# Performance work log

Hardware: AMD Instinct MI355X
Metric: run time of the kernel (lower is better)

The kernel has to match this reference:

```python
import jax, jax.numpy as jnp
import numpy as np

B = 1024
IN_SIZ = 16384
OUT_SIZ = 16384
C = 8          # channel_siz
NLVL = 10
IFS = IN_SIZ // 2 ** NLVL                                   # 16, in_filter_siz
KLVL = min(int(np.floor(np.log2(OUT_SIZ / 2))), NLVL)       # 10
OFS = OUT_SIZ // 2 ** KLVL                                  # 16, out_filter_siz
STD = 0.9


def setup_inputs() -> dict:
    key = jax.random.key(0)
    ks = jax.random.split(key, 2 * NLVL + 3)
    inp = {}
    inp["x"] = jax.random.normal(ks[0], (B, IN_SIZ, 1), jnp.float32)
    inp["in_filter"] = jax.random.normal(ks[1], (IFS, 1, C), jnp.float32) * STD
    inp["in_bias"] = jnp.zeros((C,), jnp.float32)
    for lvl in range(1, NLVL + 1):
        k = 2 ** lvl
        inp[f"W{lvl}"] = jax.random.normal(ks[2 * lvl], (k, 2, C, C), jnp.float32) * STD
        inp[f"b{lvl}"] = jnp.zeros((k, C), jnp.float32)
    inp["fea_dense"] = jax.random.normal(ks[-1], (2 ** KLVL, C, OFS), jnp.float32) * STD
    return inp


def _level(v, W, b):
    # v: [Kp, B, L, C] parent branches; W: [2*Kp, 2, C, C]; b: [2*Kp, C]
    # kernel-2 stride-2 conv1d: out[t] = relu(x[2t] @ W[0] + x[2t+1] @ W[1] + b)
    Kp, Bn, L, Cc = v.shape
    xp = v.reshape(Kp, Bn, L // 2, 2, Cc)
    xr = jnp.repeat(xp, 2, axis=0)  # child itk reads parent itk // 2
    y = jnp.einsum('kbtsc,kscd->kbtd', xr, W) + b[:, None, None, :]
    return jax.nn.relu(y)


def reference(x, in_filter, in_bias,
              W1, b1, W2, b2, W3, b3, W4, b4, W5, b5,
              W6, b6, W7, b7, W8, b8, W9, b9, W10, b10,
              fea_dense):
    Ws = [W1, W2, W3, W4, W5, W6, W7, W8, W9, W10]
    bs = [b1, b2, b3, b4, b5, b6, b7, b8, b9, b10]
    Bn = x.shape[0]
    # input conv1d: kernel=IFS, stride=IFS (non-overlapping) == blocked matmul
    xin = x[..., 0].reshape(Bn, 2 ** NLVL, IFS)                       # [B, 1024, 16]
    v = jax.nn.relu(jnp.einsum('bnf,fc->bnc', xin, in_filter[:, 0, :]) + in_bias)
    v = v[None]                                                        # [1, B, 1024, C]
    for lvl in range(NLVL):  # klvl == nlvl: all levels branch (tree doubling)
        v = _level(v, Ws[lvl], bs[lvl])
    # v: [2^klvl, B, 1, C] -> per-branch dense feature map
    out = jnp.einsum('kbc,kcf->bkf', v[:, :, 0, :], fea_dense)         # [B, 1024, OFS]
    return out.reshape(Bn, OUT_SIZ, 1)
```

## Files before the change

kernel.cpp:

```cpp
#include <hip/hip_runtime.h>

struct PrepPtrs {
  const float* W[7]; const float* Bv[7]; const float* F; const float* fb;
  const float* W8; const float* B8; const float* W9; const float* B9;
  const float* W10; const float* B10;
};

__device__ __forceinline__ int cz(int c) { return c ^ ((c >> 3) & 3); }

__device__ __forceinline__ float4 relu4(float4 a) {
  return make_float4(fmaxf(a.x,0.f), fmaxf(a.y,0.f), fmaxf(a.z,0.f), fmaxf(a.w,0.f));
}
__device__ __forceinline__ void fma4(float4& acc, float s, const float4& wv) {
  acc.x = fmaf(s, wv.x, acc.x); acc.y = fmaf(s, wv.y, acc.y);
  acc.z = fmaf(s, wv.z, acc.z); acc.w = fmaf(s, wv.w, acc.w);
}
__device__ __forceinline__ float4 add4(float4 a, float4 b) {
  return make_float4(a.x+b.x, a.y+b.y, a.z+b.z, a.w+b.w);
}

__device__ __forceinline__ float4 entApply(const float4* __restrict__ e4,
                                           float4 A0, float4 A1,
                                           float4 C0, float4 C1) {
  float4 a0 = e4[16];
  float4 a1 = make_float4(0.f, 0.f, 0.f, 0.f);
  float4 a2 = make_float4(0.f, 0.f, 0.f, 0.f);
  float4 a3 = make_float4(0.f, 0.f, 0.f, 0.f);
  fma4(a0, A0.x, e4[0]);  fma4(a1, A0.y, e4[1]);  fma4(a2, A0.z, e4[2]);  fma4(a3, A0.w, e4[3]);
  fma4(a0, A1.x, e4[4]);  fma4(a1, A1.y, e4[5]);  fma4(a2, A1.z, e4[6]);  fma4(a3, A1.w, e4[7]);
  fma4(a0, C0.x, e4[8]);  fma4(a1, C0.y, e4[9]);  fma4(a2, C0.z, e4[10]); fma4(a3, C0.w, e4[11]);
  fma4(a0, C1.x, e4[12]); fma4(a1, C1.y, e4[13]); fma4(a2, C1.z, e4[14]); fma4(a3, C1.w, e4[15]);
  return relu4(add4(add4(a0, a1), add4(a2, a3)));
}

__global__ void bfly_prep(PrepPtrs P, float* __restrict__ wt) {
  int e = blockIdx.x * 256 + threadIdx.x;
  if (e >= 4094 * 68) return;
  int ent = e / 68, r = e % 68, dd = r & 3;
  const float* Ws; const float* Bs; int th;
  if (ent < 62) {
    if (ent < 60) {
      int lvl, base;
      if (ent < 4)       { lvl = 1; base = 0;  }
      else if (ent < 12) { lvl = 2; base = 4;  }
      else if (ent < 28) { lvl = 3; base = 12; }
      else               { lvl = 4; base = 28; }
      int k = (ent - base) >> 1; th = ent & 1;
      Ws = P.W[lvl-1] + k*128; Bs = P.Bv[lvl-1] + k*8;
    } else {
      th = ent - 60; Ws = P.F; Bs = P.fb;
    }
  } else if (ent < 510) {
    int eb = ent - 62;
    int q = eb / 56, rem = eb % 56;
    int lvl, Kl, base;
    if (rem < 8)       { lvl = 5; Kl = 4;  base = 0;  }
    else if (rem < 24) { lvl = 6; Kl = 8;  base = 8;  }
    else               { lvl = 7; Kl = 16; base = 24; }
    int rr = rem - base; int lk = rr >> 1; th = rr & 1;
    int kg = q * Kl + lk;
    Ws = P.W[lvl-1] + kg*128; Bs = P.Bv[lvl-1] + kg*8;
  } else if (ent < 1022) {
    int ec = ent - 510; int k = ec >> 1; th = ec & 1;
    Ws = P.W8 + k*128; Bs = P.B8 + k*8;
  } else if (ent < 2046) {
    int ec = ent - 1022; int k = ec >> 1; th = ec & 1;
    Ws = P.W9 + k*128; Bs = P.B9 + k*8;
  } else {
    int ec = ent - 2046; int k = ec >> 1; th = ec & 1;
    Ws = P.W10 + k*128; Bs = P.B10 + k*8;
  }
  float v;
  if (r < 64) { int s = r >> 5, c = (r >> 2) & 7; v = Ws[s*64 + c*8 + th*4 + dd]; }
  else v = Bs[th*4 + dd];
  wt[ent * 80 + r] = v;
}

__global__ __launch_bounds__(256, 2) void bfly_ka(
    const float* __restrict__ x, const float* __restrict__ wt,
    float* __restrict__ st1)
{
  const int tid = threadIdx.x;
  const int T = tid & 127;
  const int bb = tid >> 7;
  const int b = blockIdx.x * 2 + bb;
  const float4* wt4 = (const float4*)wt;
  const float4* xb4 = (const float4*)x + (size_t)b * 4096 + T * 32;

  float4 s[16], n[16];

#pragma unroll
  for (int th = 0; th < 2; ++th) {
    const float4* e4 = wt4 + (60 + th) * 20;
#pragma unroll
    for (int r = 0; r < 8; ++r) {
      float4 x0 = xb4[r*4], x1 = xb4[r*4+1], x2 = xb4[r*4+2], x3 = xb4[r*4+3];
      s[r*2+th] = entApply(e4, x0, x1, x2, x3);
    }
  }
#pragma unroll
  for (int th = 0; th < 2; ++th)
#pragma unroll
    for (int k = 0; k < 2; ++k) {
      const float4* e4 = wt4 + (0 + k*2 + th) * 20;
#pragma unroll
      for (int t = 0; t < 4; ++t)
        n[(k*4+t)*2+th] = entApply(e4, s[(2*t)*2], s[(2*t)*2+1],
                                       s[(2*t+1)*2], s[(2*t+1)*2+1]);
    }
#pragma unroll
  for (int th = 0; th < 2; ++th)
#pragma unroll
    for (int k = 0; k < 4; ++k) {
      const float4* e4 = wt4 + (4 + k*2 + th) * 20;
      const int kp = k >> 1;
#pragma unroll
      for (int t = 0; t < 2; ++t)
        s[(k*2+t)*2+th] = entApply(e4, n[(kp*4+2*t)*2], n[(kp*4+2*t)*2+1],
                                       n[(kp*4+2*t+1)*2], n[(kp*4+2*t+1)*2+1]);
    }
#pragma unroll
  for (int th = 0; th < 2; ++th)
#pragma unroll
    for (int k = 0; k < 8; ++k) {
      const float4* e4 = wt4 + (12 + k*2 + th) * 20;
      const int kp = k >> 1;
      n[k*2+th] = entApply(e4, s[(kp*2)*2], s[(kp*2)*2+1],
                               s[(kp*2+1)*2], s[(kp*2+1)*2+1]);
    }
  float4* o4 = (float4*)st1;
#pragma unroll
  for (int k = 0; k < 8; ++k)
#pragma unroll
    for (int th = 0; th < 2; ++th)
      o4[((size_t)(k*2+th) * 1024 + b) * 128 + T] = n[k*2+th];
}

template<int LV>
__device__ __forceinline__ void kb_level2(float4* __restrict__ s,
                                          const float4* __restrict__ wb4,
                                          int lane, int w) {
  constexpr int Tc = 1 << (10 - LV);
  constexpr int entB = (LV == 5) ? 0 : (LV == 6) ? 8 : 24;
  int kp, bl, t;
  if constexpr (LV == 5)      { kp = w >> 2; bl = ((w & 3) << 1) | (lane >> 5); t = lane & 31; }
  else if constexpr (LV == 6) { kp = w >> 1; bl = ((w & 1) << 2) | (lane >> 4); t = lane & 15; }
  else                        { kp = w;      bl = lane >> 3;                    t = lane & 7;  }
  const int pb = bl * 256 + kp * (2 * Tc) + 2 * t;
  const int cb = cz(pb);
  const int cb1 = cb ^ 1;
  float4 A0 = s[cb],       C0 = s[cb1];
  float4 A1 = s[cb + 128], C1 = s[cb1 + 128];
#pragma unroll
  for (int kk = 0; kk < 2; ++kk) {
    float4* pD = s + cz(bl * 256 + (2 * kp + kk) * Tc + t);
#pragma unroll
    for (int th = 0; th < 2; ++th) {
      const float4* e4 = wb4 + (entB + (2 * kp + kk) * 2 + th) * 20;
      pD[th * 128] = entApply(e4, A0, A1, C0, C1);
    }
  }
}

__global__ __launch_bounds__(512, 3) void bfly_kb(
    const float* __restrict__ st1, const float* __restrict__ wt,
    float* __restrict__ st2)
{
  __shared__ float4 s0[2048];
  const int tid = threadIdx.x;
  const int q = blockIdx.x, bt = blockIdx.y;
  const int lane = tid & 63;
  const int w = __builtin_amdgcn_readfirstlane(tid >> 6);
  const float4* wt4 = (const float4*)wt;
  const float4* wb4 = wt4 + 1240 + q * 56 * 20;
  const float4* i4 = (const float4*)st1;

#pragma unroll
  for (int it = 0; it < 4; ++it) {
    int o = tid + it * 512;
    int t3 = o & 127, h = (o >> 7) & 1, bl = o >> 8;
    float4 v = i4[((size_t)(q * 2 + h) * 1024 + bt * 8 + bl) * 128 + t3];
    s0[cz(bl * 256 + h * 128 + t3)] = v;
  }
  __syncthreads();
  {
    const float4* eb = wt4 + (28 + 4 * q) * 20;
    int bl = w, t = lane;
    int pb = bl * 256 + 2 * t;
    int cb = cz(pb), cb1 = cb ^ 1;
    float4 A0 = s0[cb], C0 = s0[cb1], A1 = s0[cb + 128], C1 = s0[cb1 + 128];
#pragma unroll
    for (int kk = 0; kk < 2; ++kk) {
      float4* pD = s0 + cz(bl * 256 + kk * 64 + t);
#pragma unroll
      for (int th = 0; th < 2; ++th) {
        const float4* e4 = eb + (kk * 2 + th) * 20;
        pD[th * 128] = entApply(e4, A0, A1, C0, C1);
      }
    }
  }
  __syncthreads();
  kb_level2<5>(s0, wb4, lane, w); __syncthreads();
  kb_level2<6>(s0, wb4, lane, w); __syncthreads();
  kb_level2<7>(s0, wb4, lane, w); __syncthreads();

  float4* o4 = (float4*)st2;
#pragma unroll
  for (int it = 0; it < 4; ++it) {
    int o = tid + it * 512;
    int bl = o & 7, t7 = (o >> 3) & 7, h = (o >> 6) & 1, lk7 = o >> 7;
    float4 v = s0[cz(bl * 256 + h * 128 + lk7 * 8 + t7)];
    o4[((size_t)((16 * q + lk7) * 8 + t7) * 2 + h) * 1024 + bt * 8 + bl] = v;
  }
}

__global__ __launch_bounds__(512, 2) void bfly_kc(
    const float* __restrict__ st, const float* __restrict__ wt,
    const float* __restrict__ fea, float* __restrict__ out)
{
  __shared__ float4 sA[1024], sB[1024];
  const int tid = threadIdx.x;
  const int j = blockIdx.x, b0 = blockIdx.y * 64;
  const int bb = tid & 63;
  const int w = __builtin_amdgcn_readfirstlane(tid >> 6);
  const float4* wt4 = (const float4*)wt;

  {
    const float4* s4 = (const float4*)st;
#pragma unroll
    for (int it = 0; it < 2; ++it) {
      int idx = tid + it * 512;
      int bl = idx & 63, h = (idx >> 6) & 1, t = idx >> 7;
      sA[h * 512 + t * 64 + bl] = s4[((size_t)((j * 8 + t) * 2 + h)) * 1024 + b0 + bl];
    }
  }
  __syncthreads();

#pragma unroll
  for (int ii = 0; ii < 2; ++ii) {
    int s = w + ii * 8;
    int th = s >> 3, k = (s >> 2) & 1, t = s & 3;
    const float4* e4 = wt4 + (510 + (2 * j + k) * 2 + th) * 20;
    float4 A0 = sA[(2*t) * 64 + bb],   A1 = sA[512 + (2*t) * 64 + bb];
    float4 C0 = sA[(2*t+1) * 64 + bb], C1 = sA[512 + (2*t+1) * 64 + bb];
    sB[th * 512 + (2*t + k) * 64 + bb] = entApply(e4, A0, A1, C0, C1);
  }
  __syncthreads();
#pragma unroll
  for (int ii = 0; ii < 2; ++ii) {
    int s = w + ii * 8;
    int th = s >> 3, k9 = (s >> 1) & 3, t9 = s & 1;
    const float4* e4 = wt4 + (1022 + (4 * j + k9) * 2 + th) * 20;
    int p0 = 4 * t9 + (k9 >> 1), p1 = p0 + 2;
    float4 A0 = sB[p0 * 64 + bb], A1 = sB[512 + p0 * 64 + bb];
    float4 C0 = sB[p1 * 64 + bb], C1 = sB[512 + p1 * 64 + bb];
    sA[th * 512 + (t9 * 4 + k9) * 64 + bb] = entApply(e4, A0, A1, C0, C1);
  }
  __syncthreads();
#pragma unroll
  for (int ii = 0; ii < 2; ++ii) {
    int s = w + ii * 8;
    int th = s >> 3, k10 = s & 7;
    const float4* e4 = wt4 + (2046 + (8 * j + k10) * 2 + th) * 20;
    int p0 = k10 >> 1, p1 = p0 + 4;
    float4 A0 = sA[p0 * 64 + bb], A1 = sA[512 + p0 * 64 + bb];
    float4 C0 = sA[p1 * 64 + bb], C1 = sA[512 + p1 * 64 + bb];
    sB[th * 512 + k10 * 64 + bb] = entApply(e4, A0, A1, C0, C1);
  }
  __syncthreads();
  {
    int cc = tid & 31, bgrp = tid >> 5;
    int k = cc >> 2, fq = cc & 3;
    const float* fp = fea + (size_t)(j * 8 + k) * 128 + fq * 4;
    float4 f0 = *(const float4*)(fp);        float4 f1 = *(const float4*)(fp + 16);
    float4 f2 = *(const float4*)(fp + 32);   float4 f3 = *(const float4*)(fp + 48);
    float4 f4_ = *(const float4*)(fp + 64);  float4 f5 = *(const float4*)(fp + 80);
    float4 f6 = *(const float4*)(fp + 96);   float4 f7 = *(const float4*)(fp + 112);
#pragma unroll
    for (int it = 0; it < 4; ++it) {
      int b_l = bgrp + it * 16;
      float4 s0v = sB[k * 64 + b_l];
      float4 s1v = sB[512 + k * 64 + b_l];
      float4 a0 = make_float4(0.f,0.f,0.f,0.f), a1 = make_float4(0.f,0.f,0.f,0.f);
      float4 a2 = make_float4(0.f,0.f,0.f,0.f), a3 = make_float4(0.f,0.f,0.f,0.f);
      fma4(a0, s0v.x, f0);  fma4(a1, s0v.y, f1);
      fma4(a2, s0v.z, f2);  fma4(a3, s0v.w, f3);
      fma4(a0, s1v.x, f4_); fma4(a1, s1v.y, f5);
      fma4(a2, s1v.z, f6);  fma4(a3, s1v.w, f7);
      float4 acc = add4(add4(a0, a1), add4(a2, a3));
      *(float4*)(out + ((size_t)(b0 + b_l)) * 16384 + j * 128 + k * 16 + fq * 4) = acc;
    }
  }
}

extern "C" void kernel_launch(void* const* d_in, const int* in_sizes, int n_in,
                              void* d_out, int out_size, void* d_ws, size_t ws_size,
                              hipStream_t stream) {
  const float* x  = (const float*)d_in[0];
  PrepPtrs P;
  P.F  = (const float*)d_in[1];
  P.fb = (const float*)d_in[2];
  for (int l = 0; l < 7; ++l) {
    P.W[l]  = (const float*)d_in[3 + 2 * l];
    P.Bv[l] = (const float*)d_in[4 + 2 * l];
  }
  P.W8  = (const float*)d_in[17];
  P.B8  = (const float*)d_in[18];
  P.W9  = (const float*)d_in[19];
  P.B9  = (const float*)d_in[20];
  P.W10 = (const float*)d_in[21];
  P.B10 = (const float*)d_in[22];
  const float* fea = (const float*)d_in[23];
  float* wt  = (float*)d_ws;
  float* st2 = (float*)d_ws + 393216;
  float* st1 = (float*)d_out;
  float* out = (float*)d_out;

  bfly_prep<<<dim3(1088), dim3(256), 0, stream>>>(P, wt);
  bfly_ka<<<dim3(512), dim3(256), 0, stream>>>(x, wt, st1);
  bfly_kb<<<dim3(8, 128), dim3(512), 0, stream>>>(st1, wt, st2);
  bfly_kc<<<dim3(128, 16), dim3(512), 0, stream>>>(st2, wt, fea, out);
}
```

Baseline: 101.3 us.

## Split bfly_ka per-thread work across two waves with LDS exchange

```diff
diff --git a/kernel.cpp b/kernel.cpp
--- a/kernel.cpp
+++ b/kernel.cpp
@@ -76,25 +76,51 @@
   wt[ent * 80 + r] = v;
 }
 
-__global__ __launch_bounds__(256, 2) void bfly_ka(
+template<int U>
+__device__ __forceinline__ void ka_tail(const float4 (&s)[8], const float4 (&p)[8],
+                                        const float4* __restrict__ wt4,
+                                        float4* __restrict__ o4, int b, int T) {
+  float4 n8[8];
+#pragma unroll
+  for (int th = 0; th < 2; ++th)
+#pragma unroll
+    for (int kl = 0; kl < 4; ++kl) {
+      const float4* e4 = wt4 + (12 + 8*U + kl*2 + th) * 20;
+      constexpr int base = 4 * U;
+      const int kp2 = base + (kl >> 1) * 2;
+      float4 A0, A1, C0, C1;
+      if constexpr (U == 0) { A0 = s[kp2]; A1 = s[kp2+1]; C0 = p[kp2]; C1 = p[kp2+1]; }
+      else                  { A0 = p[kp2]; A1 = p[kp2+1]; C0 = s[kp2]; C1 = s[kp2+1]; }
+      n8[kl*2+th] = entApply(e4, A0, A1, C0, C1);
+    }
+#pragma unroll
+  for (int kl = 0; kl < 4; ++kl)
+#pragma unroll
+    for (int th = 0; th < 2; ++th)
+      o4[((size_t)((4*U + kl)*2 + th) * 1024 + b) * 128 + T] = n8[kl*2+th];
+}
+
+__global__ __launch_bounds__(256, 4) void bfly_ka(
     const float* __restrict__ x, const float* __restrict__ wt,
     float* __restrict__ st1)
 {
+  __shared__ float4 xch[2048];
   const int tid = threadIdx.x;
-  const int T = tid & 127;
-  const int bb = tid >> 7;
-  const int b = blockIdx.x * 2 + bb;
+  const int b = blockIdx.x;
+  const int lane = tid & 63;
+  const int w = __builtin_amdgcn_readfirstlane(tid >> 6);
+  const int u = w & 1;
+  const int T = lane + (w >> 1) * 64;
   const float4* wt4 = (const float4*)wt;
-  const float4* xb4 = (const float4*)x + (size_t)b * 4096 + T * 32;
-
-  float4 s[16], n[16];
-
-#pragma unroll
-  for (int th = 0; th < 2; ++th) {
-    const float4* e4 = wt4 + (60 + th) * 20;
-#pragma unroll
-    for (int r = 0; r < 8; ++r) {
-      float4 x0 = xb4[r*4], x1 = xb4[r*4+1], x2 = xb4[r*4+2], x3 = xb4[r*4+3];
+  const float4* xb4 = (const float4*)x + (size_t)b * 4096 + T * 32 + u * 16;
+
+  float4 s[8], n8[8];
+#pragma unroll
+  for (int r = 0; r < 4; ++r) {
+    float4 x0 = xb4[r*4], x1 = xb4[r*4+1], x2 = xb4[r*4+2], x3 = xb4[r*4+3];
+#pragma unroll
+    for (int th = 0; th < 2; ++th) {
+      const float4* e4 = wt4 + (60 + th) * 20;
       s[r*2+th] = entApply(e4, x0, x1, x2, x3);
     }
   }
@@ -102,11 +128,11 @@
   for (int th = 0; th < 2; ++th)
 #pragma unroll
     for (int k = 0; k < 2; ++k) {
-      const float4* e4 = wt4 + (0 + k*2 + th) * 20;
-#pragma unroll
-      for (int t = 0; t < 4; ++t)
-        n[(k*4+t)*2+th] = entApply(e4, s[(2*t)*2], s[(2*t)*2+1],
-                                       s[(2*t+1)*2], s[(2*t+1)*2+1]);
+      const float4* e4 = wt4 + (k*2 + th) * 20;
+#pragma unroll
+      for (int tl = 0; tl < 2; ++tl)
+        n8[(k*2+tl)*2+th] = entApply(e4, s[(2*tl)*2], s[(2*tl)*2+1],
+                                         s[(2*tl+1)*2], s[(2*tl+1)*2+1]);
     }
 #pragma unroll
   for (int th = 0; th < 2; ++th)
@@ -114,26 +140,21 @@
     for (int k = 0; k < 4; ++k) {
       const float4* e4 = wt4 + (4 + k*2 + th) * 20;
       const int kp = k >> 1;
-#pragma unroll
-      for (int t = 0; t < 2; ++t)
-        s[(k*2+t)*2+th] = entApply(e4, n[(kp*4+2*t)*2], n[(kp*4+2*t)*2+1],
-                                       n[(kp*4+2*t+1)*2], n[(kp*4+2*t+1)*2+1]);
-    }
-#pragma unroll
-  for (int th = 0; th < 2; ++th)
-#pragma unroll
-    for (int k = 0; k < 8; ++k) {
-      const float4* e4 = wt4 + (12 + k*2 + th) * 20;
-      const int kp = k >> 1;
-      n[k*2+th] = entApply(e4, s[(kp*2)*2], s[(kp*2)*2+1],
-                               s[(kp*2+1)*2], s[(kp*2+1)*2+1]);
-    }
+      s[k*2+th] = entApply(e4, n8[(kp*2)*2], n8[(kp*2)*2+1],
+                               n8[(kp*2+1)*2], n8[(kp*2+1)*2+1]);
+    }
+#pragma unroll
+  for (int i = 0; i < 8; ++i)
+    xch[T*16 + u*8 + (i ^ (T & 7))] = s[i];
+  __syncthreads();
+  float4 p[8];
+#pragma unroll
+  for (int i = 0; i < 8; ++i)
+    p[i] = xch[T*16 + (1-u)*8 + (i ^ (T & 7))];
+
   float4* o4 = (float4*)st1;
-#pragma unroll
-  for (int k = 0; k < 8; ++k)
-#pragma unroll
-    for (int th = 0; th < 2; ++th)
-      o4[((size_t)(k*2+th) * 1024 + b) * 128 + T] = n[k*2+th];
+  if (u == 0) ka_tail<0>(s, p, wt4, o4, b, T);
+  else        ka_tail<1>(s, p, wt4, o4, b, T);
 }
 
 template<int LV>
@@ -317,7 +338,7 @@
   float* out = (float*)d_out;
 
   bfly_prep<<<dim3(1088), dim3(256), 0, stream>>>(P, wt);
-  bfly_ka<<<dim3(512), dim3(256), 0, stream>>>(x, wt, st1);
+  bfly_ka<<<dim3(1024), dim3(256), 0, stream>>>(x, wt, st1);
   bfly_kb<<<dim3(8, 128), dim3(512), 0, stream>>>(st1, wt, st2);
   bfly_kc<<<dim3(128, 16), dim3(512), 0, stream>>>(st2, wt, fea, out);
 }
```

Measured after the change: 96.44 us. 1.05x faster.
